# Optimization experiments

Hardware: AMD Instinct MI355X
Metric: run time of the kernel (lower is better)

The kernel has to match this reference:

```python
import jax, jax.numpy as jnp
import numpy as np
import math

EMBED = 64
HEADS = 2
HEAD_DIM = EMBED // HEADS
B = 262144
EPS = 1e-5


def _linear_params(key, fan_in, fan_out):
    kw, kb = jax.random.split(key)
    bound = 1.0 / math.sqrt(fan_in)
    W = jax.random.uniform(kw, (fan_out, fan_in), jnp.float32, -bound, bound)
    b = jax.random.uniform(kb, (fan_out,), jnp.float32, -bound, bound)
    return W, b


def setup_inputs() -> dict:
    key = jax.random.key(0)
    ks = jax.random.split(key, 12)
    v1 = jax.random.normal(ks[0], (B, EMBED), jnp.float32)
    v2 = jax.random.normal(ks[1], (B, EMBED), jnp.float32)
    Wq1, bq1 = _linear_params(ks[2], EMBED, EMBED)
    Wk2, bk2 = _linear_params(ks[3], EMBED, EMBED)
    Wv2, bv2 = _linear_params(ks[4], EMBED, EMBED)
    Wo1, bo1 = _linear_params(ks[5], EMBED, EMBED)
    Wq2, bq2 = _linear_params(ks[6], EMBED, EMBED)
    Wk1, bk1 = _linear_params(ks[7], EMBED, EMBED)
    Wv1, bv1 = _linear_params(ks[8], EMBED, EMBED)
    Wo2, bo2 = _linear_params(ks[9], EMBED, EMBED)
    g1 = jnp.ones((EMBED,), jnp.float32); be1 = jnp.zeros((EMBED,), jnp.float32)
    g2 = jnp.ones((EMBED,), jnp.float32); be2 = jnp.zeros((EMBED,), jnp.float32)
    return dict(v1_embed=v1, v2_embed=v2,
                Wq1=Wq1, bq1=bq1, Wk2=Wk2, bk2=bk2, Wv2=Wv2, bv2=bv2, Wo1=Wo1, bo1=bo1,
                Wq2=Wq2, bq2=bq2, Wk1=Wk1, bk1=bk1, Wv1=Wv1, bv1=bv1, Wo2=Wo2, bo2=bo2,
                g1=g1, be1=be1, g2=g2, be2=be2)


def _lin(x, W, b):
    return x @ W.T + b


def _mha_single_token(q, k, v):
    # q,k,v: (B, EMBED); one query token, one key token per batch element.
    Bq = q.shape[0]
    Q = q.reshape(Bq, HEADS, HEAD_DIM)
    K = k.reshape(Bq, HEADS, HEAD_DIM)
    V = v.reshape(Bq, HEADS, HEAD_DIM)
    scores = jnp.sum(Q * K, axis=-1, keepdims=True) / jnp.sqrt(jnp.float32(HEAD_DIM))  # (B,H,1)
    w = jax.nn.softmax(scores[..., None], axis=-1)[..., 0]  # softmax over length-1 key axis -> 1.0
    attended = w * V  # (B,H,HEAD_DIM)
    return attended.reshape(Bq, EMBED)


def _layernorm(x, g, b):
    mu = jnp.mean(x, axis=-1, keepdims=True)
    var = jnp.mean(jnp.square(x - mu), axis=-1, keepdims=True)
    return (x - mu) * jax.lax.rsqrt(var + EPS) * g + b


def reference(v1_embed, v2_embed, Wq1, bq1, Wk2, bk2, Wv2, bv2, Wo1, bo1,
              Wq2, bq2, Wk1, bk1, Wv1, bv1, Wo2, bo2, g1, be1, g2, be2):
    # v1 attends to v2
    q1p = _lin(v1_embed, Wq1, bq1)
    k2p = _lin(v2_embed, Wk2, bk2)
    v2p = _lin(v2_embed, Wv2, bv2)
    a1 = _lin(_mha_single_token(q1p, k2p, v2p), Wo1, bo1)
    a1 = _layernorm(a1 + v1_embed, g1, be1)
    # v2 attends to v1
    q2p = _lin(v2_embed, Wq2, bq2)
    k1p = _lin(v1_embed, Wk1, bk1)
    v1p = _lin(v1_embed, Wv1, bv1)
    a2 = _lin(_mha_single_token(q2p, k1p, v1p), Wo2, bo2)
    a2 = _layernorm(a2 + v2_embed, g2, be2)
    return a1, a2
```

## Files before the change

### kernel.cpp

```cpp
#include <hip/hip_runtime.h>

typedef unsigned short u16;
typedef short v8s __attribute__((ext_vector_type(8)));
typedef float f4 __attribute__((ext_vector_type(4)));

#define NROWS 262144

__device__ __forceinline__ u16 f2bf(float f) {
  union { float f; unsigned int i; } x; x.f = f;
  unsigned int r = x.i + 0x7fffu + ((x.i >> 16) & 1u);
  return (u16)(r >> 16);
}

__global__ void fuse_weights(const float* __restrict__ Wo1, const float* __restrict__ Wv2,
                             const float* __restrict__ bv2, const float* __restrict__ bo1,
                             const float* __restrict__ Wo2, const float* __restrict__ Wv1,
                             const float* __restrict__ bv1, const float* __restrict__ bo2,
                             const float* __restrict__ g1,  const float* __restrict__ be1,
                             const float* __restrict__ g2,  const float* __restrict__ be2,
                             u16* __restrict__ M1, u16* __restrict__ M2,
                             float* __restrict__ cgb) {
  int item = blockIdx.x * 256 + threadIdx.x;
  int mat = item >> 10;
  int n   = (item >> 4) & 63;
  int k0  = (item & 15) * 4;
  const float* Wo = mat ? Wo2 : Wo1;
  const float* Wv = mat ? Wv1 : Wv2;
  float a0 = 0.f, a1 = 0.f, a2 = 0.f, a3 = 0.f;
  for (int j = 0; j < 64; ++j) {
    float w = Wo[n * 64 + j];
    f4 wv = *(const f4*)(Wv + j * 64 + k0);
    a0 += w * wv[0];
    a1 += w * wv[1];
    a2 += w * wv[2];
    a3 += w * wv[3];
  }
  u16* M = mat ? M2 : M1;
  M[n * 64 + k0 + 0] = f2bf(a0);
  M[n * 64 + k0 + 1] = f2bf(a1);
  M[n * 64 + k0 + 2] = f2bf(a2);
  M[n * 64 + k0 + 3] = f2bf(a3);
  if ((item & 15) == 0) {
    const float* bv = mat ? bv1 : bv2;
    const float* bo = mat ? bo2 : bo1;
    float s = bo[n];
    for (int j = 0; j < 64; ++j) s += Wo[n * 64 + j] * bv[j];
    cgb[mat * 64 + n] = s;
    const float* g  = mat ? g2 : g1;
    const float* be = mat ? be2 : be1;
    cgb[128 + mat * 128 + n] = g[n];
    cgb[192 + mat * 128 + n] = be[n];
  }
}

__global__ __launch_bounds__(256, 4) void xattn(
    const float* __restrict__ v1, const float* __restrict__ v2,
    const u16* __restrict__ M1, const u16* __restrict__ M2,
    const float* __restrict__ cgb,
    float* __restrict__ out1, float* __restrict__ out2) {
  const int lane = threadIdx.x & 63;
  const int wave = threadIdx.x >> 6;
  const int quad = lane >> 4;
  const int l15  = lane & 15;
  const int path = wave & 1;

  const u16*   M    = path ? M2  : M1;
  const float* xsrc = path ? v1  : v2;
  const float* rsrc = path ? v2  : v1;
  float*       outp = path ? (float*)0 : (float*)0;
  outp = path ? out2 : out1;
  const int coff = path * 64;
  const int goff = 128 + path * 128;
  const int boff = 192 + path * 128;

  v8s a[4][2];
#pragma unroll
  for (int mt = 0; mt < 4; ++mt)
#pragma unroll
    for (int ks = 0; ks < 2; ++ks)
      a[mt][ks] = *(const v8s*)(M + (mt * 16 + l15) * 64 + ks * 32 + quad * 8);

  const int unit0 = blockIdx.x * 2 + (wave >> 1);
#pragma unroll
  for (int it = 0; it < 2; ++it) {
    const int r0 = (unit0 + it * 8192) * 16;

    const float* xrow = xsrc + (size_t)(r0 + l15) * 64 + quad * 8;
    f4 x0 = *(const f4*)(xrow);
    f4 x1 = *(const f4*)(xrow + 4);
    f4 x2 = *(const f4*)(xrow + 32);
    f4 x3 = *(const f4*)(xrow + 36);
    const float* rrow = rsrc + (size_t)(r0 + l15) * 64 + quad * 4;
    f4 rv0 = *(const f4*)(rrow);
    f4 rv1 = *(const f4*)(rrow + 16);
    f4 rv2 = *(const f4*)(rrow + 32);
    f4 rv3 = *(const f4*)(rrow + 48);

    v8s b0, b1;
#pragma unroll
    for (int j = 0; j < 4; ++j) {
      b0[j]     = (short)f2bf(x0[j]);
      b0[j + 4] = (short)f2bf(x1[j]);
      b1[j]     = (short)f2bf(x2[j]);
      b1[j + 4] = (short)f2bf(x3[j]);
    }

    f4 acc[4];
#pragma unroll
    for (int mt = 0; mt < 4; ++mt) {
      f4 c = {0.f, 0.f, 0.f, 0.f};
      c = __builtin_amdgcn_mfma_f32_16x16x32_bf16(a[mt][0], b0, c, 0, 0, 0);
      c = __builtin_amdgcn_mfma_f32_16x16x32_bf16(a[mt][1], b1, c, 0, 0, 0);
      acc[mt] = c;
    }

    float vals[16];
    float sum = 0.f, sq = 0.f;
    f4 rv[4] = {rv0, rv1, rv2, rv3};
#pragma unroll
    for (int mt = 0; mt < 4; ++mt) {
      int fo = mt * 16 + quad * 4;
      f4 cf = *(const f4*)(cgb + coff + fo);
#pragma unroll
      for (int j = 0; j < 4; ++j) {
        float x = acc[mt][j] + cf[j] + rv[mt][j];
        vals[mt * 4 + j] = x;
        sum += x;
        sq  += x * x;
      }
    }
    sum += __shfl_xor(sum, 16, 64);
    sq  += __shfl_xor(sq,  16, 64);
    sum += __shfl_xor(sum, 32, 64);
    sq  += __shfl_xor(sq,  32, 64);
    float mean = sum * 0.015625f;
    float var  = sq * 0.015625f - mean * mean;
    float rstd = rsqrtf(var + 1e-5f);

    float* orow = outp + (size_t)(r0 + l15) * 64 + quad * 4;
#pragma unroll
    for (int mt = 0; mt < 4; ++mt) {
      int fo = mt * 16 + quad * 4;
      f4 g  = *(const f4*)(cgb + goff + fo);
      f4 be = *(const f4*)(cgb + boff + fo);
      f4 o;
#pragma unroll
      for (int j = 0; j < 4; ++j)
        o[j] = (vals[mt * 4 + j] - mean) * rstd * g[j] + be[j];
      __builtin_nontemporal_store(o, (f4*)(orow + mt * 16));
    }
  }
}

extern "C" void kernel_launch(void* const* d_in, const int* in_sizes, int n_in,
                              void* d_out, int out_size, void* d_ws, size_t ws_size,
                              hipStream_t stream) {
  const float* v1  = (const float*)d_in[0];
  const float* v2  = (const float*)d_in[1];
  const float* Wv2 = (const float*)d_in[6];
  const float* bv2 = (const float*)d_in[7];
  const float* Wo1 = (const float*)d_in[8];
  const float* bo1 = (const float*)d_in[9];
  const float* Wv1 = (const float*)d_in[14];
  const float* bv1 = (const float*)d_in[15];
  const float* Wo2 = (const float*)d_in[16];
  const float* bo2 = (const float*)d_in[17];
  const float* g1  = (const float*)d_in[18];
  const float* be1 = (const float*)d_in[19];
  const float* g2  = (const float*)d_in[20];
  const float* be2 = (const float*)d_in[21];

  u16* M1 = (u16*)d_ws;
  u16* M2 = M1 + 4096;
  float* cgb = (float*)((char*)d_ws + 16384);

  float* out1 = (float*)d_out;
  float* out2 = out1 + (size_t)NROWS * 64;

  fuse_weights<<<8, 256, 0, stream>>>(Wo1, Wv2, bv2, bo1, Wo2, Wv1, bv1, bo2,
                                      g1, be1, g2, be2, M1, M2, cgb);
  xattn<<<4096, 256, 0, stream>>>(v1, v2, M1, M2, cgb, out1, out2);
}
```

Before: 303.7 us.

## Double-buffer input row loads across four tiles per wave and stage constants in LDS

Each wave now handles four 16-row tiles instead of two, with the grid halved. The next tile's input loads are issued before the current tile's MFMA and layernorm work, so global-memory latency overlaps compute. The bias, gamma and beta constants are copied into shared memory once per block instead of being read from global memory on every tile. The trade-off is more registers per thread, with launch bounds lowered to 3 blocks, and fewer blocks in flight, for a kernel that is bandwidth-bound.

```diff
diff --git a/kernel.cpp b/kernel.cpp
--- a/kernel.cpp
+++ b/kernel.cpp
@@ -5,6 +5,7 @@
 typedef float f4 __attribute__((ext_vector_type(4)));
 
 #define NROWS 262144
+#define UNITS 4
 
 __device__ __forceinline__ u16 f2bf(float f) {
   union { float f; unsigned int i; } x; x.f = f;
@@ -53,7 +54,7 @@
   }
 }
 
-__global__ __launch_bounds__(256, 4) void xattn(
+__global__ __launch_bounds__(256, 3) void xattn(
     const float* __restrict__ v1, const float* __restrict__ v2,
     const u16* __restrict__ M1, const u16* __restrict__ M2,
     const float* __restrict__ cgb,
@@ -64,11 +65,14 @@
   const int l15  = lane & 15;
   const int path = wave & 1;
 
+  __shared__ float scgb[384];
+  if (threadIdx.x < 96)
+    ((f4*)scgb)[threadIdx.x] = ((const f4*)cgb)[threadIdx.x];
+
   const u16*   M    = path ? M2  : M1;
   const float* xsrc = path ? v1  : v2;
   const float* rsrc = path ? v2  : v1;
-  float*       outp = path ? (float*)0 : (float*)0;
-  outp = path ? out2 : out1;
+  float*       outp = path ? out2 : out1;
   const int coff = path * 64;
   const int goff = 128 + path * 128;
   const int boff = 192 + path * 128;
@@ -81,28 +85,42 @@
       a[mt][ks] = *(const v8s*)(M + (mt * 16 + l15) * 64 + ks * 32 + quad * 8);
 
   const int unit0 = blockIdx.x * 2 + (wave >> 1);
-#pragma unroll
-  for (int it = 0; it < 2; ++it) {
-    const int r0 = (unit0 + it * 8192) * 16;
-
-    const float* xrow = xsrc + (size_t)(r0 + l15) * 64 + quad * 8;
-    f4 x0 = *(const f4*)(xrow);
-    f4 x1 = *(const f4*)(xrow + 4);
-    f4 x2 = *(const f4*)(xrow + 32);
-    f4 x3 = *(const f4*)(xrow + 36);
-    const float* rrow = rsrc + (size_t)(r0 + l15) * 64 + quad * 4;
-    f4 rv0 = *(const f4*)(rrow);
-    f4 rv1 = *(const f4*)(rrow + 16);
-    f4 rv2 = *(const f4*)(rrow + 32);
-    f4 rv3 = *(const f4*)(rrow + 48);
+
+  f4 x0[2], x1[2], x2[2], x3[2];
+  f4 rv0[2], rv1[2], rv2[2], rv3[2];
+
+  auto stage = [&](int buf, int tile) {
+    const int rr = tile * 16;
+    const float* xrow = xsrc + (size_t)(rr + l15) * 64 + quad * 8;
+    x0[buf] = *(const f4*)(xrow);
+    x1[buf] = *(const f4*)(xrow + 4);
+    x2[buf] = *(const f4*)(xrow + 32);
+    x3[buf] = *(const f4*)(xrow + 36);
+    const float* rrow = rsrc + (size_t)(rr + l15) * 64 + quad * 4;
+    rv0[buf] = *(const f4*)(rrow);
+    rv1[buf] = *(const f4*)(rrow + 16);
+    rv2[buf] = *(const f4*)(rrow + 32);
+    rv3[buf] = *(const f4*)(rrow + 48);
+  };
+
+  stage(0, unit0);
+  __syncthreads();
+
+#pragma unroll
+  for (int it = 0; it < UNITS; ++it) {
+    const int cur = it & 1;
+    const int nxt = cur ^ 1;
+    const int r0 = (unit0 + it * 4096) * 16;
+
+    if (it + 1 < UNITS) stage(nxt, unit0 + (it + 1) * 4096);
 
     v8s b0, b1;
 #pragma unroll
     for (int j = 0; j < 4; ++j) {
-      b0[j]     = (short)f2bf(x0[j]);
-      b0[j + 4] = (short)f2bf(x1[j]);
-      b1[j]     = (short)f2bf(x2[j]);
-      b1[j + 4] = (short)f2bf(x3[j]);
+      b0[j]     = (short)f2bf(x0[cur][j]);
+      b0[j + 4] = (short)f2bf(x1[cur][j]);
+      b1[j]     = (short)f2bf(x2[cur][j]);
+      b1[j + 4] = (short)f2bf(x3[cur][j]);
     }
 
     f4 acc[4];
@@ -114,19 +132,18 @@
       acc[mt] = c;
     }
 
-    float vals[16];
     float sum = 0.f, sq = 0.f;
-    f4 rv[4] = {rv0, rv1, rv2, rv3};
 #pragma unroll
     for (int mt = 0; mt < 4; ++mt) {
-      int fo = mt * 16 + quad * 4;
-      f4 cf = *(const f4*)(cgb + coff + fo);
+      const int fo = mt * 16 + quad * 4;
+      f4 cf = *(const f4*)(scgb + coff + fo);
+      f4 rr = mt == 0 ? rv0[cur] : mt == 1 ? rv1[cur] : mt == 2 ? rv2[cur] : rv3[cur];
 #pragma unroll
       for (int j = 0; j < 4; ++j) {
-        float x = acc[mt][j] + cf[j] + rv[mt][j];
-        vals[mt * 4 + j] = x;
-        sum += x;
-        sq  += x * x;
+        float t = acc[mt][j] + cf[j] + rr[j];
+        acc[mt][j] = t;
+        sum += t;
+        sq  += t * t;
       }
     }
     sum += __shfl_xor(sum, 16, 64);
@@ -140,13 +157,13 @@
     float* orow = outp + (size_t)(r0 + l15) * 64 + quad * 4;
 #pragma unroll
     for (int mt = 0; mt < 4; ++mt) {
-      int fo = mt * 16 + quad * 4;
-      f4 g  = *(const f4*)(cgb + goff + fo);
-      f4 be = *(const f4*)(cgb + boff + fo);
+      const int fo = mt * 16 + quad * 4;
+      f4 g  = *(const f4*)(scgb + goff + fo);
+      f4 be = *(const f4*)(scgb + boff + fo);
       f4 o;
 #pragma unroll
       for (int j = 0; j < 4; ++j)
-        o[j] = (vals[mt * 4 + j] - mean) * rstd * g[j] + be[j];
+        o[j] = (acc[mt][j] - mean) * rstd * g[j] + be[j];
       __builtin_nontemporal_store(o, (f4*)(orow + mt * 16));
     }
   }
@@ -179,5 +196,5 @@
 
   fuse_weights<<<8, 256, 0, stream>>>(Wo1, Wv2, bv2, bo1, Wo2, Wv1, bv1, bo2,
                                       g1, be1, g2, be2, M1, M2, cgb);
-  xattn<<<4096, 256, 0, stream>>>(v1, v2, M1, M2, cgb, out1, out2);
-}
+  xattn<<<2048, 256, 0, stream>>>(v1, v2, M1, M2, cgb, out1, out2);
+}
```

Measured after the change: 299.6 us. No clear change (-1.3%).
